# Performance work log

Hardware: AMD Instinct MI355X
Metric: run time of the kernel (lower is better)

The kernel has to match this reference:

```python
import jax, jax.numpy as jnp
import numpy as np


def setup_inputs() -> dict:
    key = jax.random.key(0)
    k1, k2, k3, k4, k5 = jax.random.split(key, 5)
    B, N, C_IN, C_OUT, E = 4, 50000, 128, 128, 800000
    x = jax.random.normal(k1, (B, N, C_IN), dtype=jnp.float32)
    adj_indices = jax.random.randint(k2, (2, E), 0, N, dtype=jnp.int32)
    adj_values = jax.random.uniform(k3, (E,), dtype=jnp.float32)
    W = jax.random.normal(k4, (C_OUT, C_IN), dtype=jnp.float32) * (1.0 / np.sqrt(C_IN))
    b = jax.random.normal(k5, (C_OUT,), dtype=jnp.float32) * 0.01
    return {"x": x, "adj_indices": adj_indices, "adj_values": adj_values, "W": W, "b": b}


def reference(x, adj_indices, adj_values, W, b):
    # x: (B,N,C_in), adj_indices: (2,E), adj_values: (E,), W: (C_out,C_in), b: (C_out,)
    N = x.shape[1]
    row, col = adj_indices[0], adj_indices[1]
    # SpMM per batch: y[b,i,:] = sum_{e: row[e]==i} adj_values[e] * x[b, col[e], :]
    msgs = x[:, col, :] * adj_values[None, :, None]          # (B,E,C_in)
    agg = jax.vmap(lambda m: jax.ops.segment_sum(m, row, num_segments=N))(msgs)  # (B,N,C_in)
    return jnp.einsum('bnc,oc->bno', agg, W) + b              # (B,N,C_out)
```

## Files before the change

### kernel.cpp

```cpp
#include <hip/hip_runtime.h>
#include <hip/hip_bf16.h>

#define Bb 4
#define Nn 50000
#define Cc 128
#define CAP 64
#define YGB 3125

using bf16x8 = __attribute__((ext_vector_type(8))) short;
using f32x4  = __attribute__((ext_vector_type(4))) float;
using f32x2  = __attribute__((ext_vector_type(2))) float;

__device__ inline ushort f2bf(float f) {
  union { float f; unsigned u; } v; v.f = f;
  unsigned u = v.u;
  return (ushort)((u + 0x7fffu + ((u >> 16) & 1u)) >> 16);
}
__device__ inline float bf2f(ushort h) {
  union { unsigned u; float f; } v; v.u = ((unsigned)h) << 16;
  return v.f;
}

__global__ __launch_bounds__(256) void fused_k(
    const float* __restrict__ x, const float* __restrict__ W,
    const int* __restrict__ adj, const float* __restrict__ vals,
    int* __restrict__ fill, unsigned* __restrict__ bucket,
    ushort* __restrict__ y, int E, int bkb)
{
  __shared__ ushort As[64][136];
  __shared__ ushort Ws[128][136];
  int tid = threadIdx.x;

  if (blockIdx.x < bkb) {
    int e = blockIdx.x * 256 + tid;
    if (e < E) {
      int r = adj[e];
      int c = adj[E + e];
      float v = vals[e];
      int idx = atomicAdd(&fill[r], 1);
      if (idx < CAP)
        bucket[(size_t)r * CAP + idx] = ((unsigned)c << 16) | (unsigned)f2bf(v);
    }
    return;
  }

  size_t mBase = (size_t)(blockIdx.x - bkb) * 64;

  for (int i = tid; i < 128 * 32; i += 256) {
    int r = i >> 5, c4 = (i & 31) << 2;
    float4 v = *reinterpret_cast<const float4*>(W + r * 128 + c4);
    ushort4 w4; w4.x = f2bf(v.x); w4.y = f2bf(v.y); w4.z = f2bf(v.z); w4.w = f2bf(v.w);
    *reinterpret_cast<ushort4*>(&Ws[r][c4]) = w4;
  }
  for (int i = tid; i < 64 * 32; i += 256) {
    int r = i >> 5, c4 = (i & 31) << 2;
    float4 v = *reinterpret_cast<const float4*>(x + (mBase + r) * 128 + c4);
    ushort4 a4; a4.x = f2bf(v.x); a4.y = f2bf(v.y); a4.z = f2bf(v.z); a4.w = f2bf(v.w);
    *reinterpret_cast<ushort4*>(&As[r][c4]) = a4;
  }
  __syncthreads();

  int w = tid >> 6, l = tid & 63;
  int mrow = (w << 4) + (l & 15);
  int kgrp = (l >> 4) << 3;
  f32x4 acc[8];
  #pragma unroll
  for (int nf = 0; nf < 8; ++nf) acc[nf] = (f32x4){0.f, 0.f, 0.f, 0.f};

  #pragma unroll
  for (int k0 = 0; k0 < 128; k0 += 32) {
    bf16x8 a = *reinterpret_cast<const bf16x8*>(&As[mrow][k0 + kgrp]);
    #pragma unroll
    for (int nf = 0; nf < 8; ++nf) {
      bf16x8 bfr = *reinterpret_cast<const bf16x8*>(&Ws[(nf << 4) + (l & 15)][k0 + kgrp]);
      acc[nf] = __builtin_amdgcn_mfma_f32_16x16x32_bf16(a, bfr, acc[nf], 0, 0, 0);
    }
  }
  __syncthreads();

  int col = l & 15;
  int rquad = (l >> 4) << 2;
  #pragma unroll
  for (int nf = 0; nf < 8; ++nf) {
    int gcol = (nf << 4) + col;
    #pragma unroll
    for (int i = 0; i < 4; ++i)
      As[(w << 4) + rquad + i][gcol] = f2bf(acc[nf][i]);
  }
  __syncthreads();

  for (int i = tid; i < 64 * 16; i += 256) {
    int r = i >> 4, chunk = i & 15;
    unsigned m = (unsigned)(mBase + r);
    unsigned b = m / Nn, n = m % Nn;
    *reinterpret_cast<bf16x8*>(y + ((size_t)n * 4 + b) * 128 + chunk * 8) =
        *reinterpret_cast<const bf16x8*>(&As[r][chunk * 8]);
  }
}

__global__ __launch_bounds__(256) void gather_k(
    const ushort* __restrict__ y, const int* __restrict__ fill,
    const unsigned* __restrict__ bucket, const float* __restrict__ bias,
    float* __restrict__ out)
{
  int row = blockIdx.x;
  int t = threadIdx.x;
  int b = t >> 6, l = t & 63;
  int cnt = min(fill[row], CAP);
  const unsigned* bp = bucket + (size_t)row * CAP;
  const ushort* yb = y + b * 128 + 2 * l;
  float ax = 0.f, ay = 0.f;
  int k = 0;
  for (; k + 1 < cnt; k += 2) {
    unsigned p0 = bp[k], p1 = bp[k + 1];
    float v0 = bf2f((ushort)p0), v1 = bf2f((ushort)p1);
    ushort2 y0 = *reinterpret_cast<const ushort2*>(yb + (size_t)(p0 >> 16) * 512);
    ushort2 y1 = *reinterpret_cast<const ushort2*>(yb + (size_t)(p1 >> 16) * 512);
    ax += v0 * bf2f(y0.x) + v1 * bf2f(y1.x);
    ay += v0 * bf2f(y0.y) + v1 * bf2f(y1.y);
  }
  if (k < cnt) {
    unsigned p0 = bp[k];
    float v0 = bf2f((ushort)p0);
    ushort2 y0 = *reinterpret_cast<const ushort2*>(yb + (size_t)(p0 >> 16) * 512);
    ax += v0 * bf2f(y0.x);
    ay += v0 * bf2f(y0.y);
  }
  f32x2 bv = *reinterpret_cast<const f32x2*>(bias + 2 * l);
  f32x2 o; o[0] = ax + bv[0]; o[1] = ay + bv[1];
  __builtin_nontemporal_store(
      o, reinterpret_cast<f32x2*>(out + ((size_t)b * Nn + row) * Cc + 2 * l));
}

extern "C" void kernel_launch(void* const* d_in, const int* in_sizes, int n_in,
                              void* d_out, int out_size, void* d_ws, size_t ws_size,
                              hipStream_t stream) {
  const float* x    = (const float*)d_in[0];
  const int*   adj  = (const int*)d_in[1];
  const float* vals = (const float*)d_in[2];
  const float* W    = (const float*)d_in[3];
  const float* bias = (const float*)d_in[4];
  float* out = (float*)d_out;
  int E = in_sizes[2];

  char* ws = (char*)d_ws;
  int*      fill   = (int*)     (ws + 0);
  unsigned* bucket = (unsigned*)(ws + 200064);
  ushort*   y      = (ushort*)  (ws + 13000064);

  hipMemsetAsync(fill, 0, Nn * sizeof(int), stream);

  int bkb = (E + 255) / 256;
  fused_k<<<bkb + YGB, 256, 0, stream>>>(x, W, adj, vals, fill, bucket, y, E, bkb);
  gather_k<<<Nn, 256, 0, stream>>>(y, fill, bucket, bias, out);
}
```

Baseline: 373.6 us.

## Load GEMM A operand directly from global and split gather edges across wavefronts

The GEMM phase stops staging x through shared memory. Each lane now loads its A fragment straight from global memory, converts it to bf16 in registers, and reuses the W tile's LDS for the output staging, which lowers LDS use and may raise occupancy. The gather kernel switches to 16-byte loads of 8 channels per lane. The edges of a row are split across four wavefronts and combined with an LDS reduction, which adds memory-level parallelism per row at the cost of a barrier and extra shared-memory traffic.

```diff
diff --git a/kernel.cpp b/kernel.cpp
--- a/kernel.cpp
+++ b/kernel.cpp
@@ -9,7 +9,6 @@
 
 using bf16x8 = __attribute__((ext_vector_type(8))) short;
 using f32x4  = __attribute__((ext_vector_type(4))) float;
-using f32x2  = __attribute__((ext_vector_type(2))) float;
 
 __device__ inline ushort f2bf(float f) {
   union { float f; unsigned u; } v; v.f = f;
@@ -27,7 +26,6 @@
     int* __restrict__ fill, unsigned* __restrict__ bucket,
     ushort* __restrict__ y, int E, int bkb)
 {
-  __shared__ ushort As[64][136];
   __shared__ ushort Ws[128][136];
   int tid = threadIdx.x;
 
@@ -52,32 +50,34 @@
     ushort4 w4; w4.x = f2bf(v.x); w4.y = f2bf(v.y); w4.z = f2bf(v.z); w4.w = f2bf(v.w);
     *reinterpret_cast<ushort4*>(&Ws[r][c4]) = w4;
   }
-  for (int i = tid; i < 64 * 32; i += 256) {
-    int r = i >> 5, c4 = (i & 31) << 2;
-    float4 v = *reinterpret_cast<const float4*>(x + (mBase + r) * 128 + c4);
-    ushort4 a4; a4.x = f2bf(v.x); a4.y = f2bf(v.y); a4.z = f2bf(v.z); a4.w = f2bf(v.w);
-    *reinterpret_cast<ushort4*>(&As[r][c4]) = a4;
-  }
   __syncthreads();
 
   int w = tid >> 6, l = tid & 63;
-  int mrow = (w << 4) + (l & 15);
-  int kgrp = (l >> 4) << 3;
+  size_t arow = mBase + (w << 4) + (l & 15);
+  int kg = (l >> 4) << 3;
   f32x4 acc[8];
   #pragma unroll
   for (int nf = 0; nf < 8; ++nf) acc[nf] = (f32x4){0.f, 0.f, 0.f, 0.f};
 
   #pragma unroll
   for (int k0 = 0; k0 < 128; k0 += 32) {
-    bf16x8 a = *reinterpret_cast<const bf16x8*>(&As[mrow][k0 + kgrp]);
+    const float* xp = x + arow * 128 + k0 + kg;
+    float4 xa = *reinterpret_cast<const float4*>(xp);
+    float4 xc = *reinterpret_cast<const float4*>(xp + 4);
+    bf16x8 a;
+    a[0] = (short)f2bf(xa.x); a[1] = (short)f2bf(xa.y);
+    a[2] = (short)f2bf(xa.z); a[3] = (short)f2bf(xa.w);
+    a[4] = (short)f2bf(xc.x); a[5] = (short)f2bf(xc.y);
+    a[6] = (short)f2bf(xc.z); a[7] = (short)f2bf(xc.w);
     #pragma unroll
     for (int nf = 0; nf < 8; ++nf) {
-      bf16x8 bfr = *reinterpret_cast<const bf16x8*>(&Ws[(nf << 4) + (l & 15)][k0 + kgrp]);
+      bf16x8 bfr = *reinterpret_cast<const bf16x8*>(&Ws[(nf << 4) + (l & 15)][k0 + kg]);
       acc[nf] = __builtin_amdgcn_mfma_f32_16x16x32_bf16(a, bfr, acc[nf], 0, 0, 0);
     }
   }
   __syncthreads();
 
+  ushort (*Cs)[136] = reinterpret_cast<ushort (*)[136]>(Ws);
   int col = l & 15;
   int rquad = (l >> 4) << 2;
   #pragma unroll
@@ -85,7 +85,7 @@
     int gcol = (nf << 4) + col;
     #pragma unroll
     for (int i = 0; i < 4; ++i)
-      As[(w << 4) + rquad + i][gcol] = f2bf(acc[nf][i]);
+      Cs[(w << 4) + rquad + i][gcol] = f2bf(acc[nf][i]);
   }
   __syncthreads();
 
@@ -94,7 +94,7 @@
     unsigned m = (unsigned)(mBase + r);
     unsigned b = m / Nn, n = m % Nn;
     *reinterpret_cast<bf16x8*>(y + ((size_t)n * 4 + b) * 128 + chunk * 8) =
-        *reinterpret_cast<const bf16x8*>(&As[r][chunk * 8]);
+        *reinterpret_cast<const bf16x8*>(&Cs[r][chunk * 8]);
   }
 }
 
@@ -103,33 +103,46 @@
     const unsigned* __restrict__ bucket, const float* __restrict__ bias,
     float* __restrict__ out)
 {
+  __shared__ float red[3][4][16][8];
   int row = blockIdx.x;
   int t = threadIdx.x;
-  int b = t >> 6, l = t & 63;
+  int q = t >> 6;
+  int b = (t >> 4) & 3;
+  int l = t & 15;
   int cnt = min(fill[row], CAP);
   const unsigned* bp = bucket + (size_t)row * CAP;
-  const ushort* yb = y + b * 128 + 2 * l;
-  float ax = 0.f, ay = 0.f;
-  int k = 0;
-  for (; k + 1 < cnt; k += 2) {
-    unsigned p0 = bp[k], p1 = bp[k + 1];
-    float v0 = bf2f((ushort)p0), v1 = bf2f((ushort)p1);
-    ushort2 y0 = *reinterpret_cast<const ushort2*>(yb + (size_t)(p0 >> 16) * 512);
-    ushort2 y1 = *reinterpret_cast<const ushort2*>(yb + (size_t)(p1 >> 16) * 512);
-    ax += v0 * bf2f(y0.x) + v1 * bf2f(y1.x);
-    ay += v0 * bf2f(y0.y) + v1 * bf2f(y1.y);
+  const ushort* yb = y + b * 128 + l * 8;
+
+  f32x4 a0 = (f32x4){0.f, 0.f, 0.f, 0.f};
+  f32x4 a1 = (f32x4){0.f, 0.f, 0.f, 0.f};
+  #pragma unroll 2
+  for (int k = q; k < cnt; k += 4) {
+    unsigned pk = bp[k];
+    float v = bf2f((ushort)pk);
+    bf16x8 yv = *reinterpret_cast<const bf16x8*>(yb + (size_t)(pk >> 16) * 512);
+    a0[0] += v * bf2f((ushort)yv[0]); a0[1] += v * bf2f((ushort)yv[1]);
+    a0[2] += v * bf2f((ushort)yv[2]); a0[3] += v * bf2f((ushort)yv[3]);
+    a1[0] += v * bf2f((ushort)yv[4]); a1[1] += v * bf2f((ushort)yv[5]);
+    a1[2] += v * bf2f((ushort)yv[6]); a1[3] += v * bf2f((ushort)yv[7]);
   }
-  if (k < cnt) {
-    unsigned p0 = bp[k];
-    float v0 = bf2f((ushort)p0);
-    ushort2 y0 = *reinterpret_cast<const ushort2*>(yb + (size_t)(p0 >> 16) * 512);
-    ax += v0 * bf2f(y0.x);
-    ay += v0 * bf2f(y0.y);
+  if (q) {
+    *reinterpret_cast<f32x4*>(&red[q - 1][b][l][0]) = a0;
+    *reinterpret_cast<f32x4*>(&red[q - 1][b][l][4]) = a1;
   }
-  f32x2 bv = *reinterpret_cast<const f32x2*>(bias + 2 * l);
-  f32x2 o; o[0] = ax + bv[0]; o[1] = ay + bv[1];
-  __builtin_nontemporal_store(
-      o, reinterpret_cast<f32x2*>(out + ((size_t)b * Nn + row) * Cc + 2 * l));
+  __syncthreads();
+  if (q == 0) {
+    #pragma unroll
+    for (int j = 0; j < 3; ++j) {
+      a0 += *reinterpret_cast<const f32x4*>(&red[j][b][l][0]);
+      a1 += *reinterpret_cast<const f32x4*>(&red[j][b][l][4]);
+    }
+    f32x4 bv0 = *reinterpret_cast<const f32x4*>(bias + l * 8);
+    f32x4 bv1 = *reinterpret_cast<const f32x4*>(bias + l * 8 + 4);
+    a0 += bv0; a1 += bv1;
+    float* op = out + ((size_t)b * Nn + row) * Cc + l * 8;
+    __builtin_nontemporal_store(a0, reinterpret_cast<f32x4*>(op));
+    __builtin_nontemporal_store(a1, reinterpret_cast<f32x4*>(op + 4));
+  }
 }
 
 extern "C" void kernel_launch(void* const* d_in, const int* in_sizes, int n_in,
```

Result: faster. 344.8 us (-7.7%).
